# Kernel optimization log

Hardware: AMD Instinct MI355X
Metric: run time of the kernel (lower is better)

Reference implementation:

```python
import jax, jax.numpy as jnp
import numpy as np

UNITS = 2048
K = 204                 # inputs per neuron = int(units * rec_conn_density)
T = 5                   # n_refractory == n_substeps (n_delay/dt)
DT = 1.0
TAU = 20.0
TAU_A = 200.0
THR = 1.0
DAMP = 0.3
DECAY = float(np.exp(-DT / TAU))
DECAY_A = float(np.exp(-DT / TAU_A))


@jax.custom_vjp
def spike(v_sc):
    return (v_sc > 0.0).astype(v_sc.dtype)

def _spike_fwd(v_sc):
    return spike(v_sc), v_sc

def _spike_bwd(v_sc, dy):
    surrogate = DAMP * jnp.maximum(1.0 - jnp.abs(v_sc), 0.0)
    return (dy * surrogate,)

spike.defvjp(_spike_fwd, _spike_bwd)


def _causal_decay_matrices(dtype):
    t = jnp.arange(T)
    diff = t[:, None] - t[None, :]            # (T, T)
    lower = diff >= 0
    Mv = jnp.where(lower, jnp.asarray(DECAY, dtype) ** diff, 0.0).astype(dtype)
    # adaptation kernel uses exponents range(-1, T-1) reversed -> decay_a**(t-s-1)
    Ma = jnp.where(lower, jnp.asarray(DECAY_A, dtype) ** (diff - 1), 0.0).astype(dtype)
    return Mv, Ma


def setup_inputs() -> dict:
    key = jax.random.key(0)
    k1, k2, k3, k4, k5, k6 = jax.random.split(key, 6)
    B = 32
    inputs = jax.random.normal(k1, (B, T * UNITS), dtype=jnp.float32)
    v0 = jax.random.normal(k2, (B, UNITS), dtype=jnp.float32)
    a0 = jax.random.uniform(k3, (B, UNITS), dtype=jnp.float32)
    # old spike buffer: binary spikes
    z_buf0 = (jax.random.uniform(k4, (B, T * UNITS)) > 0.9).astype(jnp.float32)
    w_vals = jax.random.normal(k5, (UNITS * K,), dtype=jnp.float32) / np.sqrt(K)
    beta = jnp.full((1, UNITS), 0.18, dtype=jnp.float32)
    cols = jnp.sort(jax.random.randint(k6, (UNITS, K), 0, UNITS), axis=-1)
    return {"inputs": inputs, "v0": v0, "a0": a0, "z_buf0": z_buf0,
            "w_vals": w_vals, "beta": beta, "cols": cols}


def reference(inputs, v0, a0, z_buf0, w_vals, beta, cols):
    B = inputs.shape[0]
    i_in = inputs.reshape(B, T, UNITS)                    # (B, T, U)
    old_z = z_buf0.reshape(B, T, UNITS)                   # (B, T, U)

    # sparse recurrent current: each neuron j sums K gathered presynaptic spikes
    w2 = w_vals.reshape(UNITS, K)                         # (U, K)
    gathered = old_z[:, :, cols]                          # (B, T, U, K)
    i_rec = jnp.einsum('btuk,uk->btu', gathered, w2)      # (B, T, U)

    i_total = i_in + i_rec
    Mv, Ma = _causal_decay_matrices(i_total.dtype)

    # causal decayed sum over substeps: filtered[t] = sum_{s<=t} decay^(t-s) i[s]
    filtered_i = jnp.einsum('ts,bsu->btu', Mv, i_total)

    steps = jnp.arange(1, T + 1)
    v_decay = (DECAY ** steps).astype(i_total.dtype)      # (T,)
    a_decay = (DECAY_A ** steps).astype(i_total.dtype)
    tilde_v = v_decay[None, :, None] * v0[:, None, :] + filtered_i
    tilde_a = a_decay[None, :, None] * a0[:, None, :]

    v_sc = (tilde_v - beta[:, None, :] * tilde_a - THR) / THR
    z = spike(v_sc)

    # refractory masking
    ref_old = (jnp.cumsum(old_z[:, ::-1], axis=1)[:, ::-1] - old_z) > 0.5
    ref_new = (jnp.cumsum(z, axis=1) - z) > 0.5
    z = jnp.where(ref_new | ref_old, jnp.zeros_like(z), z)

    filtered_reset = jnp.einsum('ts,bsu->btu', Mv, z * THR)
    filtered_a_inc = jnp.einsum('ts,bsu->btu', Ma, z)

    v_buf = tilde_v - filtered_reset
    a_buf = tilde_a + filtered_a_inc
    return (z, v_buf, a_buf, v_sc)
```

## Files before the change

### kernel.cpp

```cpp
#include <hip/hip_runtime.h>

#define UNITS 2048
#define KDIM  204
#define T     5
#define BATCH 32

#define BPB   8
#define UPB   32
#define ROWB  2064

#define PD1  0.951229424500714f
#define PD2  0.9048374180359595f
#define PD3  0.8607079764250578f
#define PD4  0.8187307530779818f
#define PD5  0.7788007830714049f
#define PA1  0.9950124791926823f
#define PA2  0.9900498337491681f
#define PA3  0.9851119396030626f
#define PA4  0.9801986733067553f
#define PA5  0.9753099120283326f
#define PAM1 1.0050125208594014f

__global__ __launch_bounds__(256) void alif_pack(const float* __restrict__ zbuf,
                                                 unsigned char* __restrict__ zbyte) {
    int tid = blockIdx.x * 256 + threadIdx.x;
    int u = tid & (UNITS - 1);
    int b = tid >> 11;
    unsigned v = 0;
#pragma unroll
    for (int t = 0; t < T; ++t) {
        float z = zbuf[((size_t)b * T + t) * UNITS + u];
        v |= (z > 0.5f ? 1u : 0u) << t;
    }
    zbyte[(size_t)b * UNITS + u] = (unsigned char)v;
}

#define ACC(zz, ww)                                          \
    acc0 = fmaf((float)((zz)      & 1u), (ww), acc0);        \
    acc1 = fmaf((float)(((zz)>>1) & 1u), (ww), acc1);        \
    acc2 = fmaf((float)(((zz)>>2) & 1u), (ww), acc2);        \
    acc3 = fmaf((float)(((zz)>>3) & 1u), (ww), acc3);        \
    acc4 = fmaf((float)(((zz)>>4) & 1u), (ww), acc4);

__global__ __launch_bounds__(256) void alif_main(
    const float* __restrict__ inputs, const float* __restrict__ v0,
    const float* __restrict__ a0, const float* __restrict__ wv,
    const float* __restrict__ beta, const int* __restrict__ cols,
    const unsigned char* __restrict__ zbyte, float* __restrict__ out) {

    __shared__ unsigned char lds_z[BPB * ROWB];

    const int tid  = threadIdx.x;
    const int bx   = blockIdx.x;
    const int ublk = bx & 63;
    const int bblk = bx >> 6;
    const int u       = ublk * UPB + (tid & 31);
    const int b_local = tid >> 5;
    const int b       = bblk * BPB + b_local;

    {
        const uint4* src = (const uint4*)(zbyte + (size_t)bblk * BPB * UNITS);
#pragma unroll
        for (int i = 0; i < 4; ++i) {
            int q = tid + 256 * i;
            uint4 val = src[q];
            int row = q >> 7;
            int col = (q & 127) << 4;
            *(uint4*)(&lds_z[row * ROWB + col]) = val;
        }
    }
    __syncthreads();

    const int rowoff = b_local * ROWB;

    const int4*   cp = (const int4*)(cols + (size_t)u * KDIM);
    const float4* wp = (const float4*)(wv + (size_t)u * KDIM);
    float acc0 = 0.f, acc1 = 0.f, acc2 = 0.f, acc3 = 0.f, acc4 = 0.f;

    int4   c = cp[0];
    float4 w = wp[0];
#pragma unroll 3
    for (int kk = 0; kk < KDIM / 4 - 1; ++kk) {
        int4   cn = cp[kk + 1];
        float4 wn = wp[kk + 1];
        unsigned z0 = lds_z[rowoff + c.x];
        unsigned z1 = lds_z[rowoff + c.y];
        unsigned z2 = lds_z[rowoff + c.z];
        unsigned z3 = lds_z[rowoff + c.w];
        ACC(z0, w.x) ACC(z1, w.y) ACC(z2, w.z) ACC(z3, w.w)
        c = cn; w = wn;
    }
    {
        unsigned z0 = lds_z[rowoff + c.x];
        unsigned z1 = lds_z[rowoff + c.y];
        unsigned z2 = lds_z[rowoff + c.z];
        unsigned z3 = lds_z[rowoff + c.w];
        ACC(z0, w.x) ACC(z1, w.y) ACC(z2, w.z) ACC(z3, w.w)
    }

    const size_t base = ((size_t)b * T) * UNITS + u;
    float i0 = inputs[base + 0 * UNITS] + acc0;
    float i1 = inputs[base + 1 * UNITS] + acc1;
    float i2 = inputs[base + 2 * UNITS] + acc2;
    float i3 = inputs[base + 3 * UNITS] + acc3;
    float i4 = inputs[base + 4 * UNITS] + acc4;

    const float v0v = v0[(size_t)b * UNITS + u];
    const float a0v = a0[(size_t)b * UNITS + u];
    const float bet = beta[u];

    float f0 = i0;
    float f1 = fmaf(PD1, i0, i1);
    float f2 = PD2 * i0; f2 = fmaf(PD1, i1, f2); f2 += i2;
    float f3 = PD3 * i0; f3 = fmaf(PD2, i1, f3); f3 = fmaf(PD1, i2, f3); f3 += i3;
    float f4 = PD4 * i0; f4 = fmaf(PD3, i1, f4); f4 = fmaf(PD2, i2, f4);
    f4 = fmaf(PD1, i3, f4); f4 += i4;

    float tv0 = fmaf(PD1, v0v, f0);
    float tv1 = fmaf(PD2, v0v, f1);
    float tv2 = fmaf(PD3, v0v, f2);
    float tv3 = fmaf(PD4, v0v, f3);
    float tv4 = fmaf(PD5, v0v, f4);

    float ta0 = PA1 * a0v;
    float ta1 = PA2 * a0v;
    float ta2 = PA3 * a0v;
    float ta3 = PA4 * a0v;
    float ta4 = PA5 * a0v;

    float vsc0 = tv0 - bet * ta0 - 1.0f;
    float vsc1 = tv1 - bet * ta1 - 1.0f;
    float vsc2 = tv2 - bet * ta2 - 1.0f;
    float vsc3 = tv3 - bet * ta3 - 1.0f;
    float vsc4 = tv4 - bet * ta4 - 1.0f;

    unsigned zr = (vsc0 > 0.f ? 1u : 0u) | (vsc1 > 0.f ? 2u : 0u) |
                  (vsc2 > 0.f ? 4u : 0u) | (vsc3 > 0.f ? 8u : 0u) |
                  (vsc4 > 0.f ? 16u : 0u);
    const unsigned zob = lds_z[rowoff + u];

    float zf[T];
#pragma unroll
    for (int t = 0; t < T; ++t) {
        bool raw     = (zr >> t) & 1u;
        bool blocked = ((zr & ((1u << t) - 1u)) != 0u) || ((zob >> (t + 1)) != 0u);
        zf[t] = (raw && !blocked) ? 1.0f : 0.0f;
    }

    float r0 = zf[0];
    float r1 = fmaf(PD1, zf[0], zf[1]);
    float r2 = PD2 * zf[0]; r2 = fmaf(PD1, zf[1], r2); r2 += zf[2];
    float r3 = PD3 * zf[0]; r3 = fmaf(PD2, zf[1], r3); r3 = fmaf(PD1, zf[2], r3); r3 += zf[3];
    float r4 = PD4 * zf[0]; r4 = fmaf(PD3, zf[1], r4); r4 = fmaf(PD2, zf[2], r4);
    r4 = fmaf(PD1, zf[3], r4); r4 += zf[4];

    float g0 = PAM1 * zf[0];
    float g1 = zf[0]; g1 = fmaf(PAM1, zf[1], g1);
    float g2 = PA1 * zf[0]; g2 += zf[1]; g2 = fmaf(PAM1, zf[2], g2);
    float g3 = PA2 * zf[0]; g3 = fmaf(PA1, zf[1], g3); g3 += zf[2]; g3 = fmaf(PAM1, zf[3], g3);
    float g4 = PA3 * zf[0]; g4 = fmaf(PA2, zf[1], g4); g4 = fmaf(PA1, zf[2], g4);
    g4 += zf[3]; g4 = fmaf(PAM1, zf[4], g4);

    const size_t BTU = (size_t)BATCH * T * UNITS;
    out[0 * BTU + base + 0 * UNITS] = zf[0];
    out[0 * BTU + base + 1 * UNITS] = zf[1];
    out[0 * BTU + base + 2 * UNITS] = zf[2];
    out[0 * BTU + base + 3 * UNITS] = zf[3];
    out[0 * BTU + base + 4 * UNITS] = zf[4];
    out[1 * BTU + base + 0 * UNITS] = tv0 - r0;
    out[1 * BTU + base + 1 * UNITS] = tv1 - r1;
    out[1 * BTU + base + 2 * UNITS] = tv2 - r2;
    out[1 * BTU + base + 3 * UNITS] = tv3 - r3;
    out[1 * BTU + base + 4 * UNITS] = tv4 - r4;
    out[2 * BTU + base + 0 * UNITS] = ta0 + g0;
    out[2 * BTU + base + 1 * UNITS] = ta1 + g1;
    out[2 * BTU + base + 2 * UNITS] = ta2 + g2;
    out[2 * BTU + base + 3 * UNITS] = ta3 + g3;
    out[2 * BTU + base + 4 * UNITS] = ta4 + g4;
    out[3 * BTU + base + 0 * UNITS] = vsc0;
    out[3 * BTU + base + 1 * UNITS] = vsc1;
    out[3 * BTU + base + 2 * UNITS] = vsc2;
    out[3 * BTU + base + 3 * UNITS] = vsc3;
    out[3 * BTU + base + 4 * UNITS] = vsc4;
}

extern "C" void kernel_launch(void* const* d_in, const int* in_sizes, int n_in,
                              void* d_out, int out_size, void* d_ws, size_t ws_size,
                              hipStream_t stream) {
    const float* inputs = (const float*)d_in[0];
    const float* v0     = (const float*)d_in[1];
    const float* a0     = (const float*)d_in[2];
    const float* zbuf0  = (const float*)d_in[3];
    const float* wvals  = (const float*)d_in[4];
    const float* beta   = (const float*)d_in[5];
    const int*   cols   = (const int*)d_in[6];
    float* out = (float*)d_out;
    unsigned char* zbyte = (unsigned char*)d_ws;

    alif_pack<<<(BATCH * UNITS) / 256, 256, 0, stream>>>(zbuf0, zbyte);
    alif_main<<<256, 256, 0, stream>>>(inputs, v0, a0, wvals, beta, cols, zbyte, out);
}
```

Baseline: 85.39 us.

## Split K reduction across two threads per neuron and double grid size

Each neuron's 204-term sparse gather is now split between two lanes (26 and 25 float4 chunks), and the partial sums are combined with a cross-lane shuffle. Units per block drop from 32 to 16, so the grid grows from 256 to 512 blocks, which is meant to raise occupancy on the many CUs and shorten each thread's serial gather chain. The two lanes also split the output stores between them. In exchange, each block reloads the same 8-row LDS spike tile, so the global-to-LDS staging traffic doubles.

```diff
diff --git a/kernel.cpp b/kernel.cpp
--- a/kernel.cpp
+++ b/kernel.cpp
@@ -6,7 +6,6 @@
 #define BATCH 32
 
 #define BPB   8
-#define UPB   32
 #define ROWB  2064
 
 #define PD1  0.951229424500714f
@@ -42,6 +41,14 @@
     acc3 = fmaf((float)(((zz)>>3) & 1u), (ww), acc3);        \
     acc4 = fmaf((float)(((zz)>>4) & 1u), (ww), acc4);
 
+#define GATHER4(cc, ww)                                      \
+    {   unsigned z0 = lds_z[rowoff + (cc).x];                \
+        unsigned z1 = lds_z[rowoff + (cc).y];                \
+        unsigned z2 = lds_z[rowoff + (cc).z];                \
+        unsigned z3 = lds_z[rowoff + (cc).w];                \
+        ACC(z0, (ww).x) ACC(z1, (ww).y)                      \
+        ACC(z2, (ww).z) ACC(z3, (ww).w) }
+
 __global__ __launch_bounds__(256) void alif_main(
     const float* __restrict__ inputs, const float* __restrict__ v0,
     const float* __restrict__ a0, const float* __restrict__ wv,
@@ -52,9 +59,10 @@
 
     const int tid  = threadIdx.x;
     const int bx   = blockIdx.x;
-    const int ublk = bx & 63;
-    const int bblk = bx >> 6;
-    const int u       = ublk * UPB + (tid & 31);
+    const int ublk = bx & 127;
+    const int bblk = bx >> 7;
+    const int u       = ublk * 16 + (tid & 15);
+    const int h       = (tid >> 4) & 1;
     const int b_local = tid >> 5;
     const int b       = bblk * BPB + b_local;
 
@@ -73,30 +81,27 @@
 
     const int rowoff = b_local * ROWB;
 
-    const int4*   cp = (const int4*)(cols + (size_t)u * KDIM);
-    const float4* wp = (const float4*)(wv + (size_t)u * KDIM);
+    const int4*   cp = (const int4*)(cols + (size_t)u * KDIM) + h * 26;
+    const float4* wp = (const float4*)(wv + (size_t)u * KDIM) + h * 26;
+    const int n = 26 - h;
     float acc0 = 0.f, acc1 = 0.f, acc2 = 0.f, acc3 = 0.f, acc4 = 0.f;
 
-    int4   c = cp[0];
-    float4 w = wp[0];
-#pragma unroll 3
-    for (int kk = 0; kk < KDIM / 4 - 1; ++kk) {
-        int4   cn = cp[kk + 1];
-        float4 wn = wp[kk + 1];
-        unsigned z0 = lds_z[rowoff + c.x];
-        unsigned z1 = lds_z[rowoff + c.y];
-        unsigned z2 = lds_z[rowoff + c.z];
-        unsigned z3 = lds_z[rowoff + c.w];
-        ACC(z0, w.x) ACC(z1, w.y) ACC(z2, w.z) ACC(z3, w.w)
-        c = cn; w = wn;
-    }
-    {
-        unsigned z0 = lds_z[rowoff + c.x];
-        unsigned z1 = lds_z[rowoff + c.y];
-        unsigned z2 = lds_z[rowoff + c.z];
-        unsigned z3 = lds_z[rowoff + c.w];
-        ACC(z0, w.x) ACC(z1, w.y) ACC(z2, w.z) ACC(z3, w.w)
-    }
+    int4   c0 = cp[0];  float4 w0 = wp[0];
+    int4   c1 = cp[1];  float4 w1 = wp[1];
+    for (int kk = 0; kk < n - 2; ++kk) {
+        int4   cn = cp[kk + 2];
+        float4 wn = wp[kk + 2];
+        GATHER4(c0, w0)
+        c0 = c1; w0 = w1; c1 = cn; w1 = wn;
+    }
+    GATHER4(c0, w0)
+    GATHER4(c1, w1)
+
+    acc0 += __shfl_xor(acc0, 16);
+    acc1 += __shfl_xor(acc1, 16);
+    acc2 += __shfl_xor(acc2, 16);
+    acc3 += __shfl_xor(acc3, 16);
+    acc4 += __shfl_xor(acc4, 16);
 
     const size_t base = ((size_t)b * T) * UNITS + u;
     float i0 = inputs[base + 0 * UNITS] + acc0;
@@ -162,26 +167,29 @@
     g4 += zf[3]; g4 = fmaf(PAM1, zf[4], g4);
 
     const size_t BTU = (size_t)BATCH * T * UNITS;
-    out[0 * BTU + base + 0 * UNITS] = zf[0];
-    out[0 * BTU + base + 1 * UNITS] = zf[1];
-    out[0 * BTU + base + 2 * UNITS] = zf[2];
-    out[0 * BTU + base + 3 * UNITS] = zf[3];
-    out[0 * BTU + base + 4 * UNITS] = zf[4];
-    out[1 * BTU + base + 0 * UNITS] = tv0 - r0;
-    out[1 * BTU + base + 1 * UNITS] = tv1 - r1;
-    out[1 * BTU + base + 2 * UNITS] = tv2 - r2;
-    out[1 * BTU + base + 3 * UNITS] = tv3 - r3;
-    out[1 * BTU + base + 4 * UNITS] = tv4 - r4;
-    out[2 * BTU + base + 0 * UNITS] = ta0 + g0;
-    out[2 * BTU + base + 1 * UNITS] = ta1 + g1;
-    out[2 * BTU + base + 2 * UNITS] = ta2 + g2;
-    out[2 * BTU + base + 3 * UNITS] = ta3 + g3;
-    out[2 * BTU + base + 4 * UNITS] = ta4 + g4;
-    out[3 * BTU + base + 0 * UNITS] = vsc0;
-    out[3 * BTU + base + 1 * UNITS] = vsc1;
-    out[3 * BTU + base + 2 * UNITS] = vsc2;
-    out[3 * BTU + base + 3 * UNITS] = vsc3;
-    out[3 * BTU + base + 4 * UNITS] = vsc4;
+    if (h == 0) {
+        out[0 * BTU + base + 0 * UNITS] = zf[0];
+        out[0 * BTU + base + 1 * UNITS] = zf[1];
+        out[0 * BTU + base + 2 * UNITS] = zf[2];
+        out[0 * BTU + base + 3 * UNITS] = zf[3];
+        out[0 * BTU + base + 4 * UNITS] = zf[4];
+        out[1 * BTU + base + 0 * UNITS] = tv0 - r0;
+        out[1 * BTU + base + 1 * UNITS] = tv1 - r1;
+        out[1 * BTU + base + 2 * UNITS] = tv2 - r2;
+        out[1 * BTU + base + 3 * UNITS] = tv3 - r3;
+        out[1 * BTU + base + 4 * UNITS] = tv4 - r4;
+    } else {
+        out[2 * BTU + base + 0 * UNITS] = ta0 + g0;
+        out[2 * BTU + base + 1 * UNITS] = ta1 + g1;
+        out[2 * BTU + base + 2 * UNITS] = ta2 + g2;
+        out[2 * BTU + base + 3 * UNITS] = ta3 + g3;
+        out[2 * BTU + base + 4 * UNITS] = ta4 + g4;
+        out[3 * BTU + base + 0 * UNITS] = vsc0;
+        out[3 * BTU + base + 1 * UNITS] = vsc1;
+        out[3 * BTU + base + 2 * UNITS] = vsc2;
+        out[3 * BTU + base + 3 * UNITS] = vsc3;
+        out[3 * BTU + base + 4 * UNITS] = vsc4;
+    }
 }
 
 extern "C" void kernel_launch(void* const* d_in, const int* in_sizes, int n_in,
@@ -198,5 +206,5 @@
     unsigned char* zbyte = (unsigned char*)d_ws;
 
     alif_pack<<<(BATCH * UNITS) / 256, 256, 0, stream>>>(zbuf0, zbyte);
-    alif_main<<<256, 256, 0, stream>>>(inputs, v0, a0, wvals, beta, cols, zbyte, out);
+    alif_main<<<512, 256, 0, stream>>>(inputs, v0, a0, wvals, beta, cols, zbyte, out);
 }
```

New measurement: 79.80 us. -6.5%, faster.
